# Optimization experiments

Hardware: AMD Instinct MI355X
Metric: run time of the kernel (lower is better)

Reference implementation:

```python
import jax, jax.numpy as jnp
import numpy as np

N_NODES = 50000
N_EDGES = 400000
D = 512
LN_EPS = 1e-5


def setup_inputs() -> dict:
    key = jax.random.key(0)
    k0, k1, k2, k3 = jax.random.split(key, 4)
    x = jax.random.normal(k0, (N_NODES, D), dtype=jnp.float32)
    src = jax.random.randint(k1, (N_EDGES,), 0, N_NODES, dtype=jnp.int64)
    dst = jax.random.randint(k2, (N_EDGES,), 0, N_NODES, dtype=jnp.int64)
    W = jax.random.normal(k3, (D, D), dtype=jnp.float32) * 0.05
    b = jnp.zeros((D,), dtype=jnp.float32)
    gamma = jnp.ones((D,), dtype=jnp.float32)
    beta = jnp.zeros((D,), dtype=jnp.float32)
    return {"x": x, "W": W, "b": b, "gamma": gamma, "beta": beta, "src": src, "dst": dst}


def reference(x, W, b, gamma, beta, src, dst):
    n = x.shape[0]
    ones = jnp.ones(src.shape, dtype=x.dtype)
    # DGL GraphConv norm='both': clamp degrees to >= 1
    deg_out = jnp.clip(jax.ops.segment_sum(ones, src, num_segments=n), 1.0)  # [N]
    deg_in = jnp.clip(jax.ops.segment_sum(ones, dst, num_segments=n), 1.0)   # [N]
    h = x * jax.lax.rsqrt(deg_out)[:, None]                 # [N, D] src normalization
    agg = jax.ops.segment_sum(h[src], dst, num_segments=n)  # gather->scatter-add SpMM
    h = agg * jax.lax.rsqrt(deg_in)[:, None]                # dst normalization
    h = h @ W + b                                           # dense linear
    # LayerNorm over last dim
    mu = jnp.mean(h, axis=-1, keepdims=True)
    var = jnp.mean(jnp.square(h - mu), axis=-1, keepdims=True)
    h = (h - mu) * jax.lax.rsqrt(var + LN_EPS) * gamma + beta
    # torch nn.GELU default = exact erf GELU
    return jax.nn.gelu(h, approximate=False)
```

## Files before the change

kernel.cpp:

```cpp
#include <hip/hip_runtime.h>
#include <hip/hip_bf16.h>

#define D 512

typedef __attribute__((ext_vector_type(8))) short bf16x8;
typedef __attribute__((ext_vector_type(4))) float f32x4;

__device__ inline float b2f(short h) {
    union { unsigned u; float f; } c;
    c.u = ((unsigned)(unsigned short)h) << 16;
    return c.f;
}

__global__ void k_hist(const int* __restrict__ src, const int* __restrict__ dst,
                       int* __restrict__ deg_out, int* __restrict__ deg_in, int E) {
    int e = blockIdx.x * 256 + threadIdx.x;
    if (e < E) {
        atomicAdd(&deg_out[src[e]], 1);
        atomicAdd(&deg_in[dst[e]], 1);
    }
}

__global__ __launch_bounds__(256)
void k_scale(const float* __restrict__ x, const int* __restrict__ deg_out,
             __hip_bfloat16* __restrict__ xs, int total16) {
    int i = blockIdx.x * 256 + threadIdx.x;
    if (i >= total16) return;
    int node = i >> 6;
    float w = rsqrtf((float)max(deg_out[node], 1));
    const float4* p = (const float4*)(x + (size_t)i * 8);
    float4 a = p[0], b = p[1];
    union { float4 f4; __hip_bfloat16 h[8]; } o;
    o.h[0] = __float2bfloat16(a.x * w);
    o.h[1] = __float2bfloat16(a.y * w);
    o.h[2] = __float2bfloat16(a.z * w);
    o.h[3] = __float2bfloat16(a.w * w);
    o.h[4] = __float2bfloat16(b.x * w);
    o.h[5] = __float2bfloat16(b.y * w);
    o.h[6] = __float2bfloat16(b.z * w);
    o.h[7] = __float2bfloat16(b.w * w);
    *(float4*)(xs + (size_t)i * 8) = o.f4;
}

__global__ void k_scan1(const int* __restrict__ deg_in, int* __restrict__ row_start,
                        int* __restrict__ partials, int N) {
    __shared__ int sm[1024];
    int tid = threadIdx.x;
    int i = blockIdx.x * 1024 + tid;
    int v = (i < N) ? deg_in[i] : 0;
    sm[tid] = v;
    __syncthreads();
    int acc = v;
    #pragma unroll
    for (int off = 1; off < 1024; off <<= 1) {
        int t = (tid >= off) ? sm[tid - off] : 0;
        __syncthreads();
        acc += t;
        sm[tid] = acc;
        __syncthreads();
    }
    if (i < N) row_start[i] = acc - v;
    if (tid == 1023) partials[blockIdx.x] = acc;
}

__global__ void k_scan2w(int* __restrict__ partials, int* __restrict__ row_start,
                         int nb, int N) {
    int lane = threadIdx.x;
    int orig = (lane < nb) ? partials[lane] : 0;
    int v = orig;
    #pragma unroll
    for (int off = 1; off < 64; off <<= 1) {
        int t = __shfl_up(v, off, 64);
        if (lane >= off) v += t;
    }
    if (lane < nb) partials[lane] = v - orig;
    if (lane == 63) row_start[N] = v;
}

__global__ void k_scan2s(int* __restrict__ partials, int* __restrict__ row_start,
                         int nb, int N) {
    if (threadIdx.x == 0 && blockIdx.x == 0) {
        int run = 0;
        for (int b = 0; b < nb; b++) { int t = partials[b]; partials[b] = run; run += t; }
        row_start[N] = run;
    }
}

__global__ void k_scan3(int* __restrict__ row_start, const int* __restrict__ partials, int N) {
    int i = blockIdx.x * 256 + threadIdx.x;
    if (i < N) row_start[i] += partials[i >> 10];
}

__global__ void k_fill(const int* __restrict__ src, const int* __restrict__ dst,
                       const int* __restrict__ row_start, int* __restrict__ cursor,
                       int* __restrict__ csr_src, int E) {
    int e = blockIdx.x * 256 + threadIdx.x;
    if (e < E) {
        int d = dst[e];
        int slot = atomicAdd(&cursor[d], 1);
        csr_src[row_start[d] + slot] = src[e];
    }
}

__global__ __launch_bounds__(256)
void k_spmm(const __hip_bfloat16* __restrict__ xs, const int* __restrict__ row_start,
            const int* __restrict__ csr_src, __hip_bfloat16* __restrict__ A, int N) {
    int wid = threadIdx.x >> 6;
    int lane = threadIdx.x & 63;
    int node = blockIdx.x * 4 + wid;
    if (node >= N) return;
    int rs = row_start[node], re = row_start[node + 1];

    float acc[8];
    #pragma unroll
    for (int k = 0; k < 8; k++) acc[k] = 0.f;
    const __hip_bfloat16* xl = xs + (size_t)lane * 8;

    int j = rs;
    for (; j + 4 <= re; j += 4) {
        int s0 = csr_src[j], s1 = csr_src[j + 1], s2 = csr_src[j + 2], s3 = csr_src[j + 3];
        bf16x8 v0 = *(const bf16x8*)(xl + (size_t)s0 * D);
        bf16x8 v1 = *(const bf16x8*)(xl + (size_t)s1 * D);
        bf16x8 v2 = *(const bf16x8*)(xl + (size_t)s2 * D);
        bf16x8 v3 = *(const bf16x8*)(xl + (size_t)s3 * D);
        #pragma unroll
        for (int k = 0; k < 8; k++)
            acc[k] += (b2f(v0[k]) + b2f(v1[k])) + (b2f(v2[k]) + b2f(v3[k]));
    }
    for (; j < re; j++) {
        int s = csr_src[j];
        bf16x8 v = *(const bf16x8*)(xl + (size_t)s * D);
        #pragma unroll
        for (int k = 0; k < 8; k++) acc[k] += b2f(v[k]);
    }

    float rn = rsqrtf((float)max(re - rs, 1));
    union { float4 f4; __hip_bfloat16 h[8]; } o;
    #pragma unroll
    for (int k = 0; k < 8; k++) o.h[k] = __float2bfloat16(acc[k] * rn);
    *(float4*)(A + (size_t)node * D + lane * 8) = o.f4;
}

__global__ __launch_bounds__(256)
void k_spmm_f32(const float* __restrict__ x, const int* __restrict__ row_start,
                const int* __restrict__ csr_src, const int* __restrict__ deg_out,
                __hip_bfloat16* __restrict__ A, int N) {
    int wid = threadIdx.x >> 6;
    int lane = threadIdx.x & 63;
    int node = blockIdx.x * 4 + wid;
    if (node >= N) return;
    int rs = row_start[node], re = row_start[node + 1];
    float4 acc0 = {0.f, 0.f, 0.f, 0.f};
    float4 acc1 = {0.f, 0.f, 0.f, 0.f};
    const float* xl = x + (size_t)lane * 8;
    for (int j = rs; j < re; j++) {
        int s = csr_src[j];
        float w = rsqrtf((float)max(deg_out[s], 1));
        const float4* p = (const float4*)(xl + (size_t)s * D);
        float4 a = p[0], b = p[1];
        acc0.x += a.x * w; acc0.y += a.y * w; acc0.z += a.z * w; acc0.w += a.w * w;
        acc1.x += b.x * w; acc1.y += b.y * w; acc1.z += b.z * w; acc1.w += b.w * w;
    }
    float rn = rsqrtf((float)max(re - rs, 1));
    union { float4 f4; __hip_bfloat16 h[8]; } o;
    o.h[0] = __float2bfloat16(acc0.x * rn);
    o.h[1] = __float2bfloat16(acc0.y * rn);
    o.h[2] = __float2bfloat16(acc0.z * rn);
    o.h[3] = __float2bfloat16(acc0.w * rn);
    o.h[4] = __float2bfloat16(acc1.x * rn);
    o.h[5] = __float2bfloat16(acc1.y * rn);
    o.h[6] = __float2bfloat16(acc1.z * rn);
    o.h[7] = __float2bfloat16(acc1.w * rn);
    *(float4*)(A + (size_t)node * D + lane * 8) = o.f4;
}

__global__ void k_packw2(const float* __restrict__ W, __hip_bfloat16* __restrict__ Wp) {
    int bid = blockIdx.x;
    int c = bid >> 7, kt = (bid >> 3) & 15, ntc = bid & 7;
    int lane = threadIdx.x;
    int k0 = kt * 32 + (lane >> 4) * 8;
    int n  = (c * 8 + ntc) * 16 + (lane & 15);
    union { float4 f4; __hip_bfloat16 h[8]; } o;
    #pragma unroll
    for (int j = 0; j < 8; j++)
        o.h[j] = __float2bfloat16(W[(size_t)(k0 + j) * D + n]);
    *(float4*)(Wp + ((size_t)bid * 64 + lane) * 8) = o.f4;
}

__global__ void k_packw(const float* __restrict__ W, __hip_bfloat16* __restrict__ Wp) {
    int tile = blockIdx.x;
    int lane = threadIdx.x;
    int kt = tile >> 5, nt = tile & 31;
    int k0 = kt * 32 + (lane >> 4) * 8;
    int n  = nt * 16 + (lane & 15);
    union { float4 f4; __hip_bfloat16 h[8]; } o;
    #pragma unroll
    for (int j = 0; j < 8; j++)
        o.h[j] = __float2bfloat16(W[(size_t)(k0 + j) * D + n]);
    *(float4*)(Wp + ((size_t)tile * 64 + lane) * 8) = o.f4;
}

__global__ __launch_bounds__(512, 2)
void k_gemm4(const __hip_bfloat16* __restrict__ A, const __hip_bfloat16* __restrict__ Wp,
             const float* __restrict__ bias, const float* __restrict__ gamma,
             const float* __restrict__ beta, float* __restrict__ out, int M) {
    __shared__ float s_sum[128][4];
    __shared__ float s_sq[128][4];

    int tid = threadIdx.x;
    int wid = tid >> 6, lane = tid & 63;
    int wm = wid >> 2, wn = wid & 3;
    int l4 = lane >> 4, coll = lane & 15;
    int tb = blockIdx.x * 128;

    const char* ap[4];
    #pragma unroll
    for (int ai = 0; ai < 4; ai++) {
        int row = tb + wm * 64 + ai * 16 + coll;
        if (row > M - 1) row = M - 1;
        ap[ai] = (const char*)A + (size_t)row * 1024 + l4 * 16;
    }
    const char* wb = (const char*)Wp + ((size_t)(wn * 128) * 64 + lane) * 16;

    f32x4 acc[4][8];
    #pragma unroll
    for (int ai = 0; ai < 4; ai++)
        #pragma unroll
        for (int t = 0; t < 8; t++) acc[ai][t] = (f32x4){0.f, 0.f, 0.f, 0.f};

    for (int kt = 0; kt < 16; kt++) {
        bf16x8 af[4];
        #pragma unroll
        for (int ai = 0; ai < 4; ai++)
            af[ai] = *(const bf16x8*)(ap[ai] + (size_t)kt * 64);
        const char* wk = wb + (size_t)kt * 8192;
        bf16x8 bf[8];
        #pragma unroll
        for (int t = 0; t < 8; t++)
            bf[t] = *(const bf16x8*)(wk + (size_t)t * 1024);
        #pragma unroll
        for (int t = 0; t < 8; t++)
            #pragma unroll
            for (int ai = 0; ai < 4; ai++)
                acc[ai][t] = __builtin_amdgcn_mfma_f32_16x16x32_bf16(af[ai], bf[t], acc[ai][t], 0, 0, 0);
    }

    float bia[8], gam[8], bet[8];
    #pragma unroll
    for (int t = 0; t < 8; t++) {
        int col = wn * 128 + t * 16 + coll;
        bia[t] = bias[col]; gam[t] = gamma[col]; bet[t] = beta[col];
    }
    #pragma unroll
    for (int ai = 0; ai < 4; ai++) {
        #pragma unroll
        for (int r = 0; r < 4; r++) {
            float s = 0.f, q = 0.f;
            #pragma unroll
            for (int t = 0; t < 8; t++) {
                float v = acc[ai][t][r] + bia[t];
                acc[ai][t][r] = v;
                s += v; q += v * v;
            }
            #pragma unroll
            for (int off = 1; off < 16; off <<= 1) {
                s += __shfl_xor(s, off, 64);
                q += __shfl_xor(q, off, 64);
            }
            if (coll == 0) {
                int rb = wm * 64 + ai * 16 + l4 * 4 + r;
                s_sum[rb][wn] = s;
                s_sq[rb][wn] = q;
            }
        }
    }
    __syncthreads();

    #pragma unroll
    for (int ai = 0; ai < 4; ai++) {
        #pragma unroll
        for (int r = 0; r < 4; r++) {
            int rb = wm * 64 + ai * 16 + l4 * 4 + r;
            int gr = tb + rb;
            if (gr >= M) continue;
            float s = s_sum[rb][0] + s_sum[rb][1] + s_sum[rb][2] + s_sum[rb][3];
            float q = s_sq[rb][0] + s_sq[rb][1] + s_sq[rb][2] + s_sq[rb][3];
            float mean = s * (1.0f / 512.0f);
            float var = q * (1.0f / 512.0f) - mean * mean;
            float rstd = rsqrtf(fmaxf(var, 0.f) + 1e-5f);
            float* orow = out + (size_t)gr * D + wn * 128 + coll;
            #pragma unroll
            for (int t = 0; t < 8; t++) {
                float y = (acc[ai][t][r] - mean) * rstd * gam[t] + bet[t];
                float yy = y * y;
                float pz = fmaf(yy, -0.1029423374f, -2.3022076728f);
                float e = __builtin_amdgcn_exp2f(y * pz);
                float g = y * __builtin_amdgcn_rcpf(1.0f + e);
                orow[t * 16] = g;
            }
        }
    }
}

__global__ __launch_bounds__(512)
void k_gemm(const __hip_bfloat16* __restrict__ A, const __hip_bfloat16* __restrict__ Wp,
            const float* __restrict__ bias, const float* __restrict__ gamma,
            const float* __restrict__ beta, float* __restrict__ out, int M) {
    int tid = threadIdx.x;
    int wid = tid >> 6, lane = tid & 63;
    int wm = wid >> 2;
    int wn = wid & 3;
    int l4 = lane >> 4, coll = lane & 15;
    int m0 = blockIdx.x * 32 + wm * 16;
    int arow = m0 + coll;
    bool rowok = (arow < M);

    f32x4 acc[8];
    #pragma unroll
    for (int t = 0; t < 8; t++) acc[t] = (f32x4){0.f, 0.f, 0.f, 0.f};

    const bf16x8* wpb = (const bf16x8*)Wp;
    for (int kt = 0; kt < 16; kt++) {
        bf16x8 afrag;
        if (rowok) afrag = *(const bf16x8*)(A + (size_t)arow * D + kt * 32 + l4 * 8);
        else afrag = (bf16x8){0,0,0,0,0,0,0,0};
        const bf16x8* wp = wpb + ((size_t)(kt * 32 + wn * 8) * 64 + lane);
        #pragma unroll
        for (int t = 0; t < 8; t++) {
            bf16x8 bfrag = wp[(size_t)t * 64];
            acc[t] = __builtin_amdgcn_mfma_f32_16x16x32_bf16(afrag, bfrag, acc[t], 0, 0, 0);
        }
    }
    __shared__ float s_sum[32][4];
    __shared__ float s_sq[32][4];
    #pragma unroll
    for (int r = 0; r < 4; r++) {
        float s = 0.f, q = 0.f;
        #pragma unroll
        for (int t = 0; t < 8; t++) {
            int col = wn * 128 + t * 16 + coll;
            float v = acc[t][r] + bias[col];
            acc[t][r] = v;
            s += v; q += v * v;
        }
        #pragma unroll
        for (int off = 1; off < 16; off <<= 1) {
            s += __shfl_xor(s, off, 64);
            q += __shfl_xor(q, off, 64);
        }
        if (coll == 0) {
            int rb = wm * 16 + l4 * 4 + r;
            s_sum[rb][wn] = s;
            s_sq[rb][wn] = q;
        }
    }
    __syncthreads();
    #pragma unroll
    for (int r = 0; r < 4; r++) {
        int rb = wm * 16 + l4 * 4 + r;
        int gr = blockIdx.x * 32 + rb;
        if (gr >= M) continue;
        float s = s_sum[rb][0] + s_sum[rb][1] + s_sum[rb][2] + s_sum[rb][3];
        float q = s_sq[rb][0] + s_sq[rb][1] + s_sq[rb][2] + s_sq[rb][3];
        float mean = s * (1.0f / 512.0f);
        float var = q * (1.0f / 512.0f) - mean * mean;
        float rstd = rsqrtf(fmaxf(var, 0.f) + 1e-5f);
        #pragma unroll
        for (int t = 0; t < 8; t++) {
            int col = wn * 128 + t * 16 + coll;
            float y = (acc[t][r] - mean) * rstd * gamma[col] + beta[col];
            float yy = y * y;
            float pz = fmaf(yy, -0.1029423374f, -2.3022076728f);
            float e = __builtin_amdgcn_exp2f(y * pz);
            out[(size_t)gr * D + col] = y * __builtin_amdgcn_rcpf(1.0f + e);
        }
    }
}

extern "C" void kernel_launch(void* const* d_in, const int* in_sizes, int n_in,
                              void* d_out, int out_size, void* d_ws, size_t ws_size,
                              hipStream_t stream) {
    const float* x     = (const float*)d_in[0];
    const float* W     = (const float*)d_in[1];
    const float* b     = (const float*)d_in[2];
    const float* gamma = (const float*)d_in[3];
    const float* beta  = (const float*)d_in[4];
    const int*   src   = (const int*)d_in[5];
    const int*   dst   = (const int*)d_in[6];
    int N = in_sizes[0] / D;
    int E = in_sizes[5];
    float* out = (float*)d_out;

    int* deg_out   = (int*)d_ws;
    int* deg_in    = deg_out + N;
    int* row_start = deg_in + N;
    int* cursor    = row_start + N + 1;
    int* partials  = cursor + N;
    int* csr_src   = partials + 64;
    uintptr_t p = (uintptr_t)(csr_src + E);
    p = (p + 255) & ~(uintptr_t)255;
    __hip_bfloat16* A = (__hip_bfloat16*)p;
    p += (size_t)N * D * sizeof(__hip_bfloat16);
    p = (p + 255) & ~(uintptr_t)255;
    __hip_bfloat16* Wp = (__hip_bfloat16*)p;
    p += (size_t)D * D * sizeof(__hip_bfloat16);
    p = (p + 255) & ~(uintptr_t)255;
    __hip_bfloat16* xs = (__hip_bfloat16*)p;
    size_t need_xs = (p - (uintptr_t)d_ws) + (size_t)N * D * sizeof(__hip_bfloat16);
    bool use_bf16_path = (ws_size >= need_xs);

    hipMemsetAsync(deg_out, 0, (size_t)2 * N * sizeof(int), stream);
    hipMemsetAsync(cursor, 0, (size_t)N * sizeof(int), stream);

    k_hist<<<(E + 255) / 256, 256, 0, stream>>>(src, dst, deg_out, deg_in, E);
    int nb1 = (N + 1023) / 1024;
    k_scan1<<<nb1, 1024, 0, stream>>>(deg_in, row_start, partials, N);
    if (nb1 <= 64)
        k_scan2w<<<1, 64, 0, stream>>>(partials, row_start, nb1, N);
    else
        k_scan2s<<<1, 64, 0, stream>>>(partials, row_start, nb1, N);
    k_scan3<<<(N + 255) / 256, 256, 0, stream>>>(row_start, partials, N);
    k_fill<<<(E + 255) / 256, 256, 0, stream>>>(src, dst, row_start, cursor, csr_src, E);

    if (use_bf16_path) {
        int total16 = N * 64;
        k_scale<<<(total16 + 255) / 256, 256, 0, stream>>>(x, deg_out, xs, total16);
        k_spmm<<<(N + 3) / 4, 256, 0, stream>>>(xs, row_start, csr_src, A, N);
        k_packw2<<<512, 64, 0, stream>>>(W, Wp);
        k_gemm4<<<(N + 127) / 128, 512, 0, stream>>>(A, Wp, b, gamma, beta, out, N);
    } else {
        k_spmm_f32<<<(N + 3) / 4, 256, 0, stream>>>(x, row_start, csr_src, deg_out, A, N);
        k_packw<<<512, 64, 0, stream>>>(W, Wp);
        k_gemm<<<(N + 31) / 32, 512, 0, stream>>>(A, Wp, b, gamma, beta, out, N);
    }
}
```

Measured before the change: 250.9 us.

## Split GEMM and LayerNorm-GELU, keep W column chunk resident in LDS

The fused GEMM+LayerNorm+GELU kernel is replaced by a persistent GEMM kernel and a separate row-wise LayerNorm+GELU kernel. Each GEMM block stages a 128-column slice of packed W into 128KB of LDS once via global_load_lds, then loops over 256-row strips and writes a bf16 intermediate into the reused xs buffer. The aim is to stop re-reading W from global memory and to simplify the epilogue. The cost is an extra bf16 write and read of the full intermediate, a second launch, and low occupancy from the 128KB LDS allocation. Each wave also issues only one MFMA chain per B-fragment LDS read, and the bf16 rounding of the pre-norm values adds precision loss.

```diff
diff --git a/kernel.cpp b/kernel.cpp
--- a/kernel.cpp
+++ b/kernel.cpp
@@ -10,6 +10,11 @@
     union { unsigned u; float f; } c;
     c.u = ((unsigned)(unsigned short)h) << 16;
     return c.f;
+}
+
+__device__ __forceinline__ void stage16(const void* g, void* l) {
+    __builtin_amdgcn_global_load_lds((const __attribute__((address_space(1))) void*)g,
+                                     (__attribute__((address_space(3))) void*)l, 16, 0, 0);
 }
 
 __global__ void k_hist(const int* __restrict__ src, const int* __restrict__ dst,
@@ -200,105 +205,108 @@
     *(float4*)(Wp + ((size_t)tile * 64 + lane) * 8) = o.f4;
 }
 
-__global__ __launch_bounds__(512, 2)
-void k_gemm4(const __hip_bfloat16* __restrict__ A, const __hip_bfloat16* __restrict__ Wp,
-             const float* __restrict__ bias, const float* __restrict__ gamma,
-             const float* __restrict__ beta, float* __restrict__ out, int M) {
-    __shared__ float s_sum[128][4];
-    __shared__ float s_sq[128][4];
+__global__ __launch_bounds__(1024, 1)
+void k_gemm5(const __hip_bfloat16* __restrict__ A, const __hip_bfloat16* __restrict__ Wp,
+             __hip_bfloat16* __restrict__ h, int M) {
+    __shared__ __align__(16) char ldsW[131072];
 
     int tid = threadIdx.x;
     int wid = tid >> 6, lane = tid & 63;
-    int wm = wid >> 2, wn = wid & 3;
     int l4 = lane >> 4, coll = lane & 15;
-    int tb = blockIdx.x * 128;
-
-    const char* ap[4];
-    #pragma unroll
-    for (int ai = 0; ai < 4; ai++) {
-        int row = tb + wm * 64 + ai * 16 + coll;
-        if (row > M - 1) row = M - 1;
-        ap[ai] = (const char*)A + (size_t)row * 1024 + l4 * 16;
-    }
-    const char* wb = (const char*)Wp + ((size_t)(wn * 128) * 64 + lane) * 16;
-
-    f32x4 acc[4][8];
-    #pragma unroll
-    for (int ai = 0; ai < 4; ai++)
-        #pragma unroll
-        for (int t = 0; t < 8; t++) acc[ai][t] = (f32x4){0.f, 0.f, 0.f, 0.f};
-
-    for (int kt = 0; kt < 16; kt++) {
-        bf16x8 af[4];
-        #pragma unroll
-        for (int ai = 0; ai < 4; ai++)
-            af[ai] = *(const bf16x8*)(ap[ai] + (size_t)kt * 64);
-        const char* wk = wb + (size_t)kt * 8192;
-        bf16x8 bf[8];
-        #pragma unroll
-        for (int t = 0; t < 8; t++)
-            bf[t] = *(const bf16x8*)(wk + (size_t)t * 1024);
-        #pragma unroll
-        for (int t = 0; t < 8; t++)
-            #pragma unroll
-            for (int ai = 0; ai < 4; ai++)
-                acc[ai][t] = __builtin_amdgcn_mfma_f32_16x16x32_bf16(af[ai], bf[t], acc[ai][t], 0, 0, 0);
-    }
-
-    float bia[8], gam[8], bet[8];
-    #pragma unroll
-    for (int t = 0; t < 8; t++) {
-        int col = wn * 128 + t * 16 + coll;
-        bia[t] = bias[col]; gam[t] = gamma[col]; bet[t] = beta[col];
-    }
-    #pragma unroll
-    for (int ai = 0; ai < 4; ai++) {
-        #pragma unroll
-        for (int r = 0; r < 4; r++) {
-            float s = 0.f, q = 0.f;
+    int cch = blockIdx.x & 3;
+    int bstrip = blockIdx.x >> 2;
+
+    {
+        const char* g = (const char*)Wp + (size_t)cch * 131072 + (size_t)wid * 1024 + (size_t)lane * 16;
+        char* l = ldsW + wid * 1024;
+        #pragma unroll
+        for (int r = 0; r < 8; r++)
+            stage16(g + r * 16384, l + r * 16384);
+    }
+    asm volatile("s_waitcnt vmcnt(0)" ::: "memory");
+    __builtin_amdgcn_sched_barrier(0);
+    __builtin_amdgcn_s_barrier();
+
+    for (int sb = bstrip; ; sb += 64) {
+        int row_base = sb * 256;
+        if (row_base >= M) break;
+        int ar = row_base + wid * 16 + coll;
+        if (ar > M - 1) ar = M - 1;
+        const char* ap = (const char*)A + (size_t)ar * 1024 + l4 * 16;
+
+        f32x4 acc[8];
+        #pragma unroll
+        for (int t = 0; t < 8; t++) acc[t] = (f32x4){0.f, 0.f, 0.f, 0.f};
+
+        for (int kt = 0; kt < 16; kt++) {
+            bf16x8 af = *(const bf16x8*)(ap + (size_t)kt * 64);
+            const char* wk = ldsW + (size_t)kt * 8192 + (size_t)lane * 16;
             #pragma unroll
             for (int t = 0; t < 8; t++) {
-                float v = acc[ai][t][r] + bia[t];
-                acc[ai][t][r] = v;
-                s += v; q += v * v;
+                bf16x8 bf = *(const bf16x8*)(wk + (size_t)t * 1024);
+                acc[t] = __builtin_amdgcn_mfma_f32_16x16x32_bf16(af, bf, acc[t], 0, 0, 0);
             }
-            #pragma unroll
-            for (int off = 1; off < 16; off <<= 1) {
-                s += __shfl_xor(s, off, 64);
-                q += __shfl_xor(q, off, 64);
+        }
+
+        int rowb = row_base + wid * 16 + l4 * 4;
+        #pragma unroll
+        for (int r = 0; r < 4; r++) {
+            int row = rowb + r;
+            if (row < M) {
+                __hip_bfloat16* hrow = h + (size_t)row * D + cch * 128 + coll;
+                #pragma unroll
+                for (int t = 0; t < 8; t++)
+                    hrow[t * 16] = __float2bfloat16(acc[t][r]);
             }
-            if (coll == 0) {
-                int rb = wm * 64 + ai * 16 + l4 * 4 + r;
-                s_sum[rb][wn] = s;
-                s_sq[rb][wn] = q;
-            }
-        }
-    }
-    __syncthreads();
-
-    #pragma unroll
-    for (int ai = 0; ai < 4; ai++) {
-        #pragma unroll
-        for (int r = 0; r < 4; r++) {
-            int rb = wm * 64 + ai * 16 + l4 * 4 + r;
-            int gr = tb + rb;
-            if (gr >= M) continue;
-            float s = s_sum[rb][0] + s_sum[rb][1] + s_sum[rb][2] + s_sum[rb][3];
-            float q = s_sq[rb][0] + s_sq[rb][1] + s_sq[rb][2] + s_sq[rb][3];
-            float mean = s * (1.0f / 512.0f);
-            float var = q * (1.0f / 512.0f) - mean * mean;
-            float rstd = rsqrtf(fmaxf(var, 0.f) + 1e-5f);
-            float* orow = out + (size_t)gr * D + wn * 128 + coll;
-            #pragma unroll
-            for (int t = 0; t < 8; t++) {
-                float y = (acc[ai][t][r] - mean) * rstd * gam[t] + bet[t];
-                float yy = y * y;
-                float pz = fmaf(yy, -0.1029423374f, -2.3022076728f);
-                float e = __builtin_amdgcn_exp2f(y * pz);
-                float g = y * __builtin_amdgcn_rcpf(1.0f + e);
-                orow[t * 16] = g;
-            }
-        }
+        }
+    }
+}
+
+__global__ __launch_bounds__(256)
+void k_lngelu(const __hip_bfloat16* __restrict__ h, const float* __restrict__ bias,
+              const float* __restrict__ gamma, const float* __restrict__ beta,
+              float* __restrict__ out, int M) {
+    int gw = (blockIdx.x * 256 + threadIdx.x) >> 6;
+    int lane = threadIdx.x & 63;
+    int nw = (gridDim.x * 256) >> 6;
+
+    float g8[8], b8[8], bi8[8];
+    #pragma unroll
+    for (int k = 0; k < 8; k++) {
+        g8[k] = gamma[lane * 8 + k];
+        b8[k] = beta[lane * 8 + k];
+        bi8[k] = bias[lane * 8 + k];
+    }
+
+    for (int row = gw; row < M; row += nw) {
+        bf16x8 v = *(const bf16x8*)(h + (size_t)row * D + lane * 8);
+        float f[8];
+        float s = 0.f, q = 0.f;
+        #pragma unroll
+        for (int k = 0; k < 8; k++) {
+            f[k] = b2f(v[k]) + bi8[k];
+            s += f[k]; q += f[k] * f[k];
+        }
+        #pragma unroll
+        for (int off = 1; off < 64; off <<= 1) {
+            s += __shfl_xor(s, off, 64);
+            q += __shfl_xor(q, off, 64);
+        }
+        float mean = s * (1.0f / 512.0f);
+        float var = q * (1.0f / 512.0f) - mean * mean;
+        float rstd = rsqrtf(fmaxf(var, 0.f) + 1e-5f);
+        float o[8];
+        #pragma unroll
+        for (int k = 0; k < 8; k++) {
+            float y = (f[k] - mean) * rstd * g8[k] + b8[k];
+            float yy = y * y;
+            float pz = fmaf(yy, -0.1029423374f, -2.3022076728f);
+            float e = __builtin_amdgcn_exp2f(y * pz);
+            o[k] = y * __builtin_amdgcn_rcpf(1.0f + e);
+        }
+        float* orow = out + (size_t)row * D + lane * 8;
+        *(float4*)orow = (float4){o[0], o[1], o[2], o[3]};
+        *(float4*)(orow + 4) = (float4){o[4], o[5], o[6], o[7]};
     }
 }
 
@@ -427,7 +435,9 @@
         k_scale<<<(total16 + 255) / 256, 256, 0, stream>>>(x, deg_out, xs, total16);
         k_spmm<<<(N + 3) / 4, 256, 0, stream>>>(xs, row_start, csr_src, A, N);
         k_packw2<<<512, 64, 0, stream>>>(W, Wp);
-        k_gemm4<<<(N + 127) / 128, 512, 0, stream>>>(A, Wp, b, gamma, beta, out, N);
+        __hip_bfloat16* h = xs;
+        k_gemm5<<<256, 1024, 0, stream>>>(A, Wp, h, N);
+        k_lngelu<<<1024, 256, 0, stream>>>(h, b, gamma, beta, out, N);
     } else {
         k_spmm_f32<<<(N + 3) / 4, 256, 0, stream>>>(x, row_start, csr_src, deg_out, A, N);
         k_packw<<<512, 64, 0, stream>>>(W, Wp);
```

After: 708.8 us. 2.83x slower.
